# Kernel tuning notes

Hardware: AMD Instinct MI355X
Metric: run time of the kernel (lower is better)

The kernel has to match this reference:

```python
import jax, jax.numpy as jnp
import numpy as np

B, C, H, W = 8, 256, 64, 64
N = 3  # num_param
EPS = 1e-5


def conv2d(x, w, b=None, stride=(1, 1), padding=((0, 0), (0, 0)), dilation=(1, 1), groups=1):
    out = jax.lax.conv_general_dilated(
        x, w, window_strides=stride, padding=padding, rhs_dilation=dilation,
        dimension_numbers=('NCHW', 'OIHW', 'NCHW'), feature_group_count=groups)
    if b is not None:
        out = out + b[None, :, None, None]
    return out


def akconv(x, p_w, p_b, ak_w, ak_gamma, ak_beta):
    b, c, h, w = x.shape
    offset = conv2d(x, p_w, p_b, padding=((1, 1), (1, 1)))  # (b, 2N, h, w)
    # initial kernel offsets p_n for num_param=3: rows [0,0,1], cols [0,1,0]
    p_n = jnp.concatenate([jnp.array([0., 0., 1.]), jnp.array([0., 1., 0.])]).reshape(1, 2 * N, 1, 1)
    gx = jnp.broadcast_to(jnp.arange(h, dtype=x.dtype)[:, None], (h, w))
    gy = jnp.broadcast_to(jnp.arange(w, dtype=x.dtype)[None, :], (h, w))
    p_0 = jnp.concatenate([jnp.tile(gx[None, None], (1, N, 1, 1)),
                           jnp.tile(gy[None, None], (1, N, 1, 1))], axis=1)  # (1, 2N, h, w)
    p = p_0 + p_n + offset                      # (b, 2N, h, w)
    p = jnp.transpose(p, (0, 2, 3, 1))          # (b, h, w, 2N)
    q = jnp.floor(jax.lax.stop_gradient(p))
    q_lt_x = jnp.clip(q[..., :N], 0, h - 1)
    q_lt_y = jnp.clip(q[..., N:], 0, w - 1)
    q_rb_x = jnp.clip(q[..., :N] + 1, 0, h - 1)
    q_rb_y = jnp.clip(q[..., N:] + 1, 0, w - 1)
    px = jnp.clip(p[..., :N], 0, h - 1)
    py = jnp.clip(p[..., N:], 0, w - 1)
    # bilinear weights (b, h, w, N)
    g_lt = (1 + (q_lt_x - px)) * (1 + (q_lt_y - py))
    g_rb = (1 - (q_rb_x - px)) * (1 - (q_rb_y - py))
    g_lb = (1 + (q_lt_x - px)) * (1 - (q_rb_y - py))
    g_rt = (1 - (q_rb_x - px)) * (1 + (q_lt_y - py))

    x_flat = x.reshape(b, c, h * w)

    def gather(qx, qy):
        idx = (qx * w + qy).astype(jnp.int32).reshape(b, -1)  # (b, h*w*N)
        out = jnp.take_along_axis(x_flat, idx[:, None, :], axis=2)
        return out.reshape(b, c, h, w, N)

    x_off = (g_lt[:, None] * gather(q_lt_x, q_lt_y)
             + g_rb[:, None] * gather(q_rb_x, q_rb_y)
             + g_lb[:, None] * gather(q_lt_x, q_rb_y)
             + g_rt[:, None] * gather(q_rb_x, q_lt_y))   # (b, c, h, w, N)
    # rearrange 'b c h w n -> b c (h n) w'
    x_off = jnp.transpose(x_off, (0, 1, 2, 4, 3)).reshape(b, c, h * N, w)
    out = conv2d(x_off, ak_w, None, stride=(N, 1))        # (b, c, h, w)
    # BatchNorm2d in training mode (batch statistics) + SiLU
    mean = out.mean(axis=(0, 2, 3), keepdims=True)
    var = ((out - mean) ** 2).mean(axis=(0, 2, 3), keepdims=True)
    out = (out - mean) / jnp.sqrt(var + EPS) * ak_gamma[None, :, None, None] + ak_beta[None, :, None, None]
    return jax.nn.silu(out)


def lka(x, w0, b0, ws, bs, w1, b1):
    u = x
    attn = conv2d(x, w0, b0, padding=((2, 2), (2, 2)), groups=C)                       # 5x5 depthwise
    attn = conv2d(attn, ws, bs, padding=((9, 9), (9, 9)), dilation=(3, 3), groups=C)   # 7x7 dw, dil 3
    attn = conv2d(attn, w1, b1)                                                        # 1x1
    return u * attn


def setup_inputs() -> dict:
    key = jax.random.key(0)
    ks = jax.random.split(key, 8)
    return {
        'x': jax.random.normal(ks[0], (B, C, H, W), jnp.float32),
        'p_w': jax.random.normal(ks[1], (2 * N, C, 3, 3), jnp.float32) * 0.01,
        'p_b': jnp.zeros((2 * N,), jnp.float32),
        'ak_w': jax.random.normal(ks[2], (C, C, 3, 1), jnp.float32) * 0.05,
        'ak_gamma': jnp.ones((C,), jnp.float32),
        'ak_beta': jnp.zeros((C,), jnp.float32),
        'lka0_w': jax.random.normal(ks[3], (C, 1, 5, 5), jnp.float32) * 0.05,
        'lka0_b': jnp.zeros((C,), jnp.float32),
        'lkas_w': jax.random.normal(ks[4], (C, 1, 7, 7), jnp.float32) * 0.05,
        'lkas_b': jnp.zeros((C,), jnp.float32),
        'lka1_w': jax.random.normal(ks[5], (C, C, 1, 1), jnp.float32) * 0.05,
        'lka1_b': jnp.zeros((C,), jnp.float32),
        'conv_w': jax.random.normal(ks[6], (C, C, 1, 1), jnp.float32) * 0.05,
        'conv_b': jnp.zeros((C,), jnp.float32),
    }


def reference(x, p_w, p_b, ak_w, ak_gamma, ak_beta, lka0_w, lka0_b, lkas_w, lkas_b, lka1_w, lka1_b, conv_w, conv_b):
    res = x
    y = akconv(x, p_w, p_b, ak_w, ak_gamma, ak_beta)
    y = lka(y, lka0_w, lka0_b, lkas_w, lkas_b, lka1_w, lka1_b)
    y = conv2d(y, conv_w, conv_b)
    return y + res
```

## Files before the change

### kernel.cpp

```cpp
#include <hip/hip_runtime.h>
#include <math.h>
#include <stdint.h>

#define B_ 8
#define C_ 256
#define HW_ 4096
#define NPIX 32768
#define NELEM (B_*C_*HW_)

typedef __attribute__((ext_vector_type(8))) short short8;
typedef __attribute__((ext_vector_type(4))) float f32x4;

__device__ __forceinline__ unsigned short f2bf(float f) {
    union { float f; uint32_t u; } v; v.f = f;
    uint32_t r = v.u + 0x7FFFu + ((v.u >> 16) & 1u);
    return (unsigned short)(r >> 16);
}
__device__ __forceinline__ float b2f(unsigned short h) {
    union { uint32_t u; float f; } v; v.u = ((uint32_t)h) << 16; return v.f;
}
__device__ __forceinline__ float silu_f(float v) { return v / (1.f + __expf(-v)); }

__device__ __forceinline__ float4 up4(uint2 v) {
    float4 r;
    r.x = b2f((unsigned short)(v.x & 0xffffu));
    r.y = b2f((unsigned short)(v.x >> 16));
    r.z = b2f((unsigned short)(v.y & 0xffffu));
    r.w = b2f((unsigned short)(v.y >> 16));
    return r;
}

__device__ __forceinline__ void gl2lds16(const void* g, void* l) {
    __builtin_amdgcn_global_load_lds(
        (const __attribute__((address_space(1))) void*)g,
        (__attribute__((address_space(3))) void*)l,
        16, 0, 0);
}

__global__ __launch_bounds__(256) void prep_transpose_kernel(
    const float* __restrict__ akw, const float* __restrict__ l1w,
    const float* __restrict__ cvw, const float* __restrict__ pw,
    unsigned short* __restrict__ wak, unsigned short* __restrict__ wl1,
    unsigned short* __restrict__ wcv, float* __restrict__ pwt,
    const float* __restrict__ x, unsigned short* __restrict__ xt)
{
    __shared__ float tile[64 * 132];
    int blk = blockIdx.x;
    int tid = threadIdx.x;
    if (blk < 1024) {
        int b = blk & 7;
        int rest = blk >> 3;
        int half = rest & 1, i = rest >> 1;
        int bi = b * 64 + i;
        {
            int ci_l = tid >> 6, jj = tid & 63;
            const float* ip = x + ((size_t)b * C_ + half * 128 + ci_l) * HW_ + i * 64 + jj;
            #pragma unroll 4
            for (int it = 0; it < 32; ++it)
                tile[jj * 132 + ci_l + it * 4] = ip[(size_t)it * 4 * HW_];
        }
        __syncthreads();
        {
            int j = tid >> 2, q = tid & 3;
            unsigned short* op = xt + ((size_t)(bi * 64 + j)) * 256 + half * 128 + q * 32;
            const float* tp = &tile[j * 132 + q * 32];
            #pragma unroll
            for (int f = 0; f < 4; ++f) {
                union { unsigned short h[8]; uint4 u; } pk;
                #pragma unroll
                for (int e = 0; e < 8; ++e) pk.h[e] = f2bf(tp[f * 8 + e]);
                *(uint4*)(op + f * 8) = pk.u;
            }
        }
        return;
    }
    int gid = (blk - 1024) * 256 + tid;
    if (gid < 196608) {
        int e = gid & 7;
        int co = (gid >> 3) & 255;
        int q = gid >> 11;
        int kpp = q * 8 + e;
        int n = kpp >> 8, ci = kpp & 255;
        wak[gid] = f2bf(akw[co * 768 + ci * 3 + n]);
    }
    else if (gid < 262144) {
        int g = gid - 196608;
        int e = g & 7, co = (g >> 3) & 255, q = g >> 11;
        wl1[g] = f2bf(l1w[co * 256 + q * 8 + e]);
    }
    else if (gid < 327680) {
        int g = gid - 262144;
        int e = g & 7, co = (g >> 3) & 255, q = g >> 11;
        wcv[g] = f2bf(cvw[co * 256 + q * 8 + e]);
    }
    else if (gid < 346112) {
        int idx = gid - 327680;
        int ci = idx / 72, r = idx - ci * 72;
        int tt = r / 12, t9 = r - tt * 12;
        pwt[idx] = (t9 < 9) ? pw[tt * 2304 + ci * 9 + t9] : 0.f;
    }
}

__global__ __launch_bounds__(256) void offset_s1_kernel(
    const float* __restrict__ x, const float* __restrict__ pwt,
    float* __restrict__ part)
{
    int blk = blockIdx.x;
    int b = blk & 7;
    int rest = blk >> 3;
    int g = rest & 7, i = rest >> 3;
    int bi = b * 64 + i;
    int tid = threadIdx.x;

    __shared__ float tile[6600];

    {
        int cs = tid >> 3, r8 = tid & 7;
        const float* xp = x + ((size_t)b * C_ + g * 32 + cs) * HW_;
        #pragma unroll
        for (int t = 0; t < 6; ++t) {
            int idx = r8 * 6 + t;
            int r = idx >> 4, v4 = idx & 15;
            int ii = i + r - 1;
            float4 val = make_float4(0.f, 0.f, 0.f, 0.f);
            if (ii >= 0 && ii < 64)
                val = *(const float4*)(xp + ii * 64 + v4 * 4);
            int base = (r * 66 + 1 + v4 * 4) * 33 + cs;
            tile[base]      = val.x;  tile[base + 33]  = val.y;
            tile[base + 66] = val.z;  tile[base + 99]  = val.w;
        }
        if (tid < 192) {
            int ci = tid / 6, rem = tid - ci * 6;
            int ki = rem >> 1, side = rem & 1;
            tile[(ki * 66 + side * 65) * 33 + ci] = 0.f;
        }
    }
    __syncthreads();

    int sub = tid >> 4;
    int jq  = tid & 15;

    float acc[6][4];
    #pragma unroll
    for (int tt = 0; tt < 6; ++tt)
        #pragma unroll
        for (int p = 0; p < 4; ++p) acc[tt][p] = 0.f;

    #pragma unroll
    for (int t = 0; t < 2; ++t) {
        int ci = sub + 16 * t;
        float xv[3][6];
        #pragma unroll
        for (int ki = 0; ki < 3; ++ki)
            #pragma unroll
            for (int cc = 0; cc < 6; ++cc)
                xv[ki][cc] = tile[(ki * 66 + jq * 4 + cc) * 33 + ci];
        const float* wp = pwt + (g * 32 + ci) * 72;
        #pragma unroll
        for (int tt = 0; tt < 6; ++tt) {
            float w[9];
            *(float4*)&w[0] = *(const float4*)(wp + tt * 12);
            *(float4*)&w[4] = *(const float4*)(wp + tt * 12 + 4);
            w[8] = wp[tt * 12 + 8];
            #pragma unroll
            for (int ki = 0; ki < 3; ++ki)
                #pragma unroll
                for (int kj = 0; kj < 3; ++kj) {
                    float wgt = w[ki * 3 + kj];
                    #pragma unroll
                    for (int p = 0; p < 4; ++p)
                        acc[tt][p] += wgt * xv[ki][kj + p];
                }
        }
    }

    __syncthreads();
    {
        float* s2 = tile + sub * 387;
        #pragma unroll
        for (int tt = 0; tt < 6; ++tt)
            #pragma unroll
            for (int p = 0; p < 4; ++p)
                s2[tt * 64 + jq * 4 + p] = acc[tt][p];
    }
    __syncthreads();
    size_t pslot = (size_t)bi * 8 + g;
    for (int idx = tid; idx < 384; idx += 256) {
        float s = 0.f;
        #pragma unroll
        for (int sb = 0; sb < 16; ++sb)
            s += tile[sb * 387 + idx];
        part[pslot * 384 + idx] = s;
    }
}

__global__ __launch_bounds__(256) void offset_s2_kernel(
    const float* __restrict__ part, const float* __restrict__ pb,
    int2* __restrict__ tbl_off, float4* __restrict__ tbl_w)
{
    int pix = blockIdx.x * 256 + threadIdx.x;
    int b = pix >> 12, rem = pix & 4095, i = rem >> 6, j = rem & 63;
    int bi = b * 64 + i;
    float v[6];
    #pragma unroll
    for (int tt = 0; tt < 6; ++tt) v[tt] = pb[tt];
    for (int g = 0; g < 8; ++g) {
        const float* pp = part + ((size_t)bi * 8 + g) * 384;
        #pragma unroll
        for (int tt = 0; tt < 6; ++tt) v[tt] += pp[tt * 64 + j];
    }
    const float pnx[3] = {0.f, 0.f, 1.f};
    const float pny[3] = {0.f, 1.f, 0.f};
    #pragma unroll
    for (int n = 0; n < 3; ++n) {
        float px_ = (float)i + pnx[n] + v[n];
        float py_ = (float)j + pny[n] + v[n + 3];
        float qx = floorf(px_), qy = floorf(py_);
        float qlx = fminf(fmaxf(qx,       0.f), 63.f);
        float qly = fminf(fmaxf(qy,       0.f), 63.f);
        float qrx = fminf(fmaxf(qx + 1.f, 0.f), 63.f);
        float qry = fminf(fmaxf(qy + 1.f, 0.f), 63.f);
        float pxc = fminf(fmaxf(px_,      0.f), 63.f);
        float pyc = fminf(fmaxf(py_,      0.f), 63.f);
        float glt = (1.f + (qlx - pxc)) * (1.f + (qly - pyc));
        float grb = (1.f - (qrx - pxc)) * (1.f - (qry - pyc));
        float glb = (1.f + (qlx - pxc)) * (1.f - (qry - pyc));
        float grt = (1.f - (qrx - pxc)) * (1.f + (qly - pyc));
        int ilx = (int)qlx, irx = (int)qrx;
        int ily = (int)qly, iry = (int)qry;
        int c0; float a0, a1, b0, b1;
        if (ily == iry) {
            if (ily == 0) { c0 = 0;  a0 = glt + glb; a1 = 0.f; b0 = grt + grb; b1 = 0.f; }
            else          { c0 = 62; a0 = 0.f; a1 = glt + glb; b0 = 0.f; b1 = grt + grb; }
        } else { c0 = ily; a0 = glt; a1 = glb; b0 = grt; b1 = grb; }
        int oi = (b * 3 + n) * HW_ + i * 64 + j;
        tbl_off[oi] = make_int2(ilx * 64 + c0, irx * 64 + c0);
        tbl_w[oi]   = make_float4(a0, a1, b0, b1);
    }
}

__global__ __launch_bounds__(256) void gather_kernel(
    const unsigned short* __restrict__ xt, const int2* __restrict__ tbl_off,
    const float4* __restrict__ tbl_w, unsigned short* __restrict__ v)
{
    int blk = blockIdx.x;
    int b = blk & 7;
    int rest = blk >> 3;
    int n = rest >> 6, i = rest & 63;
    int bi = b * 64 + i;
    int tid = threadIdx.x;
    int lane = tid & 63, wv = tid >> 6;
    int ci4 = lane * 4;
    const unsigned short* xb = xt + (size_t)b * 1048576;

    __shared__ unsigned short stile[16640];
    int tCloc = ci4 >> 5;
    int kq = (ci4 >> 3) & 3;
    int e  = ci4 & 7;
    unsigned short* sl = &stile[tCloc * 2080 + kq * 520 + e];

    for (int it0 = 0; it0 < 16; it0 += 8) {
        uint2 A8[8], B8[8], C8[8], D8[8];
        float4 w4[8];
        #pragma unroll
        for (int u = 0; u < 8; ++u) {
            int j = wv * 16 + it0 + u;
            int oi = (b * 3 + n) * HW_ + i * 64 + j;
            int2 off = tbl_off[oi];
            w4[u] = tbl_w[oi];
            const unsigned short* p0 = xb + (size_t)off.x * 256 + ci4;
            const unsigned short* p1 = xb + (size_t)off.y * 256 + ci4;
            A8[u] = *(const uint2*)p0;
            B8[u] = *(const uint2*)(p0 + 256);
            C8[u] = *(const uint2*)p1;
            D8[u] = *(const uint2*)(p1 + 256);
        }
        #pragma unroll
        for (int u = 0; u < 8; ++u) {
            int j = wv * 16 + it0 + u;
            float4 A = up4(A8[u]), Bv = up4(B8[u]), Cv = up4(C8[u]), Dv = up4(D8[u]);
            union { unsigned short h[4]; uint2 q; } pk;
            pk.h[0] = f2bf(w4[u].x*A.x + w4[u].y*Bv.x + w4[u].z*Cv.x + w4[u].w*Dv.x);
            pk.h[1] = f2bf(w4[u].x*A.y + w4[u].y*Bv.y + w4[u].z*Cv.y + w4[u].w*Dv.y);
            pk.h[2] = f2bf(w4[u].x*A.z + w4[u].y*Bv.z + w4[u].z*Cv.z + w4[u].w*Dv.z);
            pk.h[3] = f2bf(w4[u].x*A.w + w4[u].y*Bv.w + w4[u].z*Cv.w + w4[u].w*Dv.w);
            *(uint2*)&sl[j * 8] = pk.q;
        }
    }
    __syncthreads();
    unsigned short* vb = v + ((size_t)bi * 24 + n * 8) * 2048;
    int kqW = tid >> 6, jW = tid & 63;
    #pragma unroll
    for (int tc = 0; tc < 8; ++tc) {
        *(uint4*)&vb[tc * 2048 + kqW * 512 + jW * 8] =
            *(const uint4*)&stile[tc * 2080 + kqW * 520 + jW * 8];
    }
}

__global__ __launch_bounds__(256) void ak_mfma_kernel(
    const unsigned short* __restrict__ v, const unsigned short* __restrict__ W,
    unsigned short* __restrict__ yh, float* __restrict__ p1, float* __restrict__ p2)
{
    int pid = blockIdx.x;
    int mt2 = (pid >> 3) & 1;
    int rest = (pid & 7) | ((pid >> 4) << 3);
    int b = rest & 7, i = rest >> 3;
    int co0 = mt2 * 128;
    int tid = threadIdx.x;
    int wv = tid >> 6, lane = tid & 63;
    int quad = lane >> 4, l15 = lane & 15;
    __shared__ __align__(16) unsigned short sA[4096];
    __shared__ __align__(16) unsigned short sB[2048];

    const unsigned short* vP = v + (size_t)(b * 64 + i) * 24 * 2048;
    int cS = tid & 127, hS = tid >> 7;

    f32x4 acc[2][4];
    #pragma unroll
    for (int mt = 0; mt < 2; ++mt)
        #pragma unroll
        for (int nt = 0; nt < 4; ++nt) acc[mt][nt] = (f32x4){0.f, 0.f, 0.f, 0.f};

    for (int t = 0; t < 24; ++t) {
        #pragma unroll
        for (int s = 0; s < 2; ++s) {
            int chunk = hS * 2 + s;
            gl2lds16(W + ((size_t)(t * 4 + chunk) * 256 + co0 + cS) * 8,
                     &sA[(chunk * 128 + cS) * 8]);
        }
        gl2lds16(vP + (size_t)t * 2048 + tid * 8, &sB[tid * 8]);
        __syncthreads();
        short8 af[2], bf[4];
        #pragma unroll
        for (int mt = 0; mt < 2; ++mt)
            af[mt] = *(const short8*)&sA[(quad * 128 + wv * 32 + mt * 16 + l15) * 8];
        #pragma unroll
        for (int nt = 0; nt < 4; ++nt)
            bf[nt] = *(const short8*)&sB[(quad * 64 + nt * 16 + l15) * 8];
        #pragma unroll
        for (int mt = 0; mt < 2; ++mt)
            #pragma unroll
            for (int nt = 0; nt < 4; ++nt)
                acc[mt][nt] = __builtin_amdgcn_mfma_f32_16x16x32_bf16(
                    af[mt], bf[nt], acc[mt][nt], 0, 0, 0);
        __syncthreads();
    }
    #pragma unroll
    for (int mt = 0; mt < 2; ++mt) {
        #pragma unroll
        for (int r = 0; r < 4; ++r) {
            int co = co0 + wv * 32 + mt * 16 + quad * 4 + r;
            size_t base = ((size_t)b * C_ + co) * HW_ + i * 64;
            float s1 = 0.f, s2 = 0.f;
            #pragma unroll
            for (int nt = 0; nt < 4; ++nt) {
                float val = acc[mt][nt][r];
                s1 += val; s2 += val * val;
                yh[base + nt * 16 + l15] = f2bf(val);
            }
            #pragma unroll
            for (int m = 1; m < 16; m <<= 1) {
                s1 += __shfl_xor(s1, m); s2 += __shfl_xor(s2, m);
            }
            if (l15 == 0) { p1[co * 512 + rest] = s1; p2[co * 512 + rest] = s2; }
        }
    }
}

__global__ __launch_bounds__(256) void bn_stats_kernel(
    const float* __restrict__ p1, const float* __restrict__ p2,
    const float* __restrict__ gamma, const float* __restrict__ beta,
    float* __restrict__ ss)
{
    int co = blockIdx.x, tid = threadIdx.x;
    float a = p1[co * 512 + tid] + p1[co * 512 + 256 + tid];
    float q = p2[co * 512 + tid] + p2[co * 512 + 256 + tid];
    __shared__ float r1[256], r2[256];
    r1[tid] = a; r2[tid] = q; __syncthreads();
    for (int st = 128; st > 0; st >>= 1) {
        if (tid < st) { r1[tid] += r1[tid + st]; r2[tid] += r2[tid + st]; }
        __syncthreads();
    }
    if (tid == 0) {
        const float inv_n = 1.f / (float)NPIX;
        float m = r1[0] * inv_n;
        float var = r2[0] * inv_n - m * m;
        float sc = gamma[co] * rsqrtf(var + 1e-5f);
        ss[co] = sc; ss[256 + co] = beta[co] - m * sc;
    }
}

__global__ __launch_bounds__(256) void dw5_fused_kernel(
    const unsigned short* __restrict__ in, const float* __restrict__ ss,
    const float* __restrict__ w, const float* __restrict__ bias,
    unsigned short* __restrict__ out)
{
    int blkI = blockIdx.x;
    int b = blkI & 7, c = blkI >> 3;
    int bc = b * 256 + c;
    int tid = threadIdx.x;
    __shared__ float tile[68 * 68];
    float sc = ss[c], sh = ss[256 + c];
    const unsigned short* ip = in + (size_t)bc * HW_;
    for (int s = tid; s < 68 * 68; s += 256) {
        int r = s / 68, cc = s - r * 68;
        int ii = r - 2, jj = cc - 2;
        float vv = 0.f;
        if (ii >= 0 && ii < 64 && jj >= 0 && jj < 64) {
            float t = b2f(ip[ii * 64 + jj]) * sc + sh;
            vv = silu_f(t);
        }
        tile[s] = vv;
    }
    float wr[25];
    #pragma unroll
    for (int t = 0; t < 25; ++t) wr[t] = w[c * 25 + t];
    float bv = bias[c];
    __syncthreads();

    int jb = tid & 3, row = tid >> 2;
    int j0 = jb * 16;
    float acc[16];
    #pragma unroll
    for (int j = 0; j < 16; ++j) acc[j] = bv;
    #pragma unroll
    for (int di = 0; di < 5; ++di) {
        const float* tp = &tile[(row + di) * 68 + j0];
        float vv[20];
        #pragma unroll
        for (int q = 0; q < 5; ++q)
            *(float4*)&vv[q * 4] = *(const float4*)(tp + q * 4);
        #pragma unroll
        for (int dj = 0; dj < 5; ++dj) {
            float wv = wr[di * 5 + dj];
            #pragma unroll
            for (int j = 0; j < 16; ++j)
                acc[j] += wv * vv[dj + j];
        }
    }
    unsigned short* op = out + (size_t)bc * HW_ + row * 64 + j0;
    union { unsigned short h[8]; uint4 u; } pk;
    #pragma unroll
    for (int half = 0; half < 2; ++half) {
        #pragma unroll
        for (int j = 0; j < 8; ++j) pk.h[j] = f2bf(acc[half * 8 + j]);
        *(uint4*)&op[half * 8] = pk.u;
    }
}

__global__ __launch_bounds__(256) void dw7d3_kernel(
    const unsigned short* __restrict__ in, const float* __restrict__ w,
    const float* __restrict__ bias, unsigned short* __restrict__ out)
{
    int blkI = blockIdx.x;
    int b = blkI & 7, c = blkI >> 3;
    int bc = b * 256 + c;
    int tid = threadIdx.x;
    __shared__ float tile[82 * 84];
    const unsigned short* ip = in + (size_t)bc * HW_;
    for (int s = tid; s < 82 * 84; s += 256) {
        int r = s / 84, cc = s - r * 84;
        int ii = r - 9, jj = cc - 9;
        float vv = 0.f;
        if (ii >= 0 && ii < 64 && jj >= 0 && jj < 64) vv = b2f(ip[ii * 64 + jj]);
        tile[s] = vv;
    }
    float wr[49];
    #pragma unroll
    for (int t = 0; t < 49; ++t) wr[t] = w[c * 49 + t];
    float bv = bias[c];
    __syncthreads();

    int jb = tid & 3, row = tid >> 2;
    int j0 = jb * 16;
    float acc[16];
    #pragma unroll
    for (int j = 0; j < 16; ++j) acc[j] = bv;
    #pragma unroll
    for (int di = 0; di < 7; ++di) {
        const float* tp = &tile[(row + 3 * di) * 84 + j0];
        float vv[36];
        #pragma unroll
        for (int q = 0; q < 9; ++q)
            *(float4*)&vv[q * 4] = *(const float4*)(tp + q * 4);
        #pragma unroll
        for (int dj = 0; dj < 7; ++dj) {
            float wv = wr[di * 7 + dj];
            #pragma unroll
            for (int j = 0; j < 16; ++j)
                acc[j] += wv * vv[3 * dj + j];
        }
    }
    unsigned short* op = out + (size_t)bc * HW_ + row * 64 + j0;
    union { unsigned short h[8]; uint4 u; } pk;
    #pragma unroll
    for (int half = 0; half < 2; ++half) {
        #pragma unroll
        for (int j = 0; j < 8; ++j) pk.h[j] = f2bf(acc[half * 8 + j]);
        *(uint4*)&op[half * 8] = pk.u;
    }
}

__global__ __launch_bounds__(256) void gemm_fused_kernel(
    const unsigned short* __restrict__ in,
    const unsigned short* __restrict__ W0, const float* __restrict__ bias0,
    const unsigned short* __restrict__ W1, const float* __restrict__ bias1,
    const unsigned short* __restrict__ auxh, const float* __restrict__ ss,
    const float* __restrict__ auxf, float* __restrict__ out_f)
{
    int blk = blockIdx.x;
    int b = blk & 7, i = blk >> 3;
    int tid = threadIdx.x;
    int wv = tid >> 6, lane = tid & 63;
    int quad = lane >> 4, l15 = lane & 15;
    __shared__ __align__(16) unsigned short sA[8192];
    __shared__ __align__(16) unsigned short sB[2048];
    __shared__ __align__(16) unsigned short mid[16384];
    int pixS = tid & 63, kqS = tid >> 6;

    const unsigned short* bp = in + ((size_t)b * C_) * HW_ + i * 64 + pixS;

    f32x4 acc[4][4];
    #pragma unroll
    for (int mt = 0; mt < 4; ++mt)
        #pragma unroll
        for (int nt = 0; nt < 4; ++nt) acc[mt][nt] = (f32x4){0.f, 0.f, 0.f, 0.f};

    for (int t = 0; t < 8; ++t) {
        #pragma unroll
        for (int s = 0; s < 4; ++s)
            gl2lds16(W0 + ((size_t)(t * 4 + s) * 256 + tid) * 8, &sA[(s * 256 + tid) * 8]);
        {
            const unsigned short* p = bp + (size_t)(t * 32 + kqS * 8) * HW_;
            union { unsigned short h[8]; uint4 u; } hb;
            #pragma unroll
            for (int jj = 0; jj < 8; ++jj) hb.h[jj] = p[(size_t)jj * HW_];
            *(uint4*)&sB[(kqS * 64 + pixS) * 8] = hb.u;
        }
        __syncthreads();
        short8 af[4], bf[4];
        #pragma unroll
        for (int mt = 0; mt < 4; ++mt)
            af[mt] = *(const short8*)&sA[(quad * 256 + wv * 64 + mt * 16 + l15) * 8];
        #pragma unroll
        for (int nt = 0; nt < 4; ++nt)
            bf[nt] = *(const short8*)&sB[(quad * 64 + nt * 16 + l15) * 8];
        #pragma unroll
        for (int mt = 0; mt < 4; ++mt)
            #pragma unroll
            for (int nt = 0; nt < 4; ++nt)
                acc[mt][nt] = __builtin_amdgcn_mfma_f32_16x16x32_bf16(
                    af[mt], bf[nt], acc[mt][nt], 0, 0, 0);
        __syncthreads();
    }
    #pragma unroll
    for (int mt = 0; mt < 4; ++mt) {
        #pragma unroll
        for (int r = 0; r < 4; ++r) {
            int co = wv * 64 + mt * 16 + quad * 4 + r;
            float bco = bias0[co];
            size_t base = ((size_t)b * C_ + co) * HW_ + i * 64;
            float sc = ss[co], sh = ss[256 + co];
            #pragma unroll
            for (int nt = 0; nt < 4; ++nt) {
                int col = nt * 16 + l15;
                float o = acc[mt][nt][r] + bco;
                float u = silu_f(b2f(auxh[base + col]) * sc + sh);
                mid[((co >> 3) * 64 + col) * 8 + (co & 7)] = f2bf(o * u);
            }
        }
    }
    #pragma unroll
    for (int mt = 0; mt < 4; ++mt)
        #pragma unroll
        for (int nt = 0; nt < 4; ++nt) acc[mt][nt] = (f32x4){0.f, 0.f, 0.f, 0.f};
    for (int t = 0; t < 8; ++t) {
        #pragma unroll
        for (int s = 0; s < 4; ++s)
            gl2lds16(W1 + ((size_t)(t * 4 + s) * 256 + tid) * 8, &sA[(s * 256 + tid) * 8]);
        __syncthreads();
        short8 af[4], bf[4];
        #pragma unroll
        for (int mt = 0; mt < 4; ++mt)
            af[mt] = *(const short8*)&sA[(quad * 256 + wv * 64 + mt * 16 + l15) * 8];
        #pragma unroll
        for (int nt = 0; nt < 4; ++nt)
            bf[nt] = *(const short8*)&mid[((t * 4 + quad) * 64 + nt * 16 + l15) * 8];
        #pragma unroll
        for (int mt = 0; mt < 4; ++mt)
            #pragma unroll
            for (int nt = 0; nt < 4; ++nt)
                acc[mt][nt] = __builtin_amdgcn_mfma_f32_16x16x32_bf16(
                    af[mt], bf[nt], acc[mt][nt], 0, 0, 0);
        __syncthreads();
    }
    #pragma unroll
    for (int mt = 0; mt < 4; ++mt) {
        #pragma unroll
        for (int r = 0; r < 4; ++r) {
            int co = wv * 64 + mt * 16 + quad * 4 + r;
            float bco = bias1[co];
            size_t base = ((size_t)b * C_ + co) * HW_ + i * 64;
            #pragma unroll
            for (int nt = 0; nt < 4; ++nt) {
                int col = nt * 16 + l15;
                out_f[base + col] = acc[mt][nt][r] + bco + auxf[base + col];
            }
        }
    }
}

extern "C" void kernel_launch(void* const* d_in, const int* in_sizes, int n_in,
                              void* d_out, int out_size, void* d_ws, size_t ws_size,
                              hipStream_t stream) {
    const float* x     = (const float*)d_in[0];
    const float* p_w   = (const float*)d_in[1];
    const float* p_b   = (const float*)d_in[2];
    const float* ak_w  = (const float*)d_in[3];
    const float* ak_g  = (const float*)d_in[4];
    const float* ak_b  = (const float*)d_in[5];
    const float* l0_w  = (const float*)d_in[6];
    const float* l0_b  = (const float*)d_in[7];
    const float* ls_w  = (const float*)d_in[8];
    const float* ls_b  = (const float*)d_in[9];
    const float* l1_w  = (const float*)d_in[10];
    const float* l1_b  = (const float*)d_in[11];
    const float* cv_w  = (const float*)d_in[12];
    const float* cv_b  = (const float*)d_in[13];
    float* out = (float*)d_out;

    char* w = (char*)d_ws;
    int2*   tbl_off = (int2*)w;
    float4* tbl_w   = (float4*)(w + 786432);
    unsigned short* wak = (unsigned short*)(w + 2359296);
    unsigned short* wl1 = (unsigned short*)(w + 2752512);
    unsigned short* wcv = (unsigned short*)(w + 2883584);
    float* p1 = (float*)(w + 3014656);
    float* p2 = (float*)(w + 3538944);
    float* ss = (float*)(w + 4063232);
    float* pwt = (float*)(w + 4065280);
    unsigned short* xt = (unsigned short*)(w + 4194304);
    unsigned short* ybh    = (unsigned short*)(w + 4194304);
    unsigned short* dw5out = (unsigned short*)(w + 20971520);
    float* part = (float*)(w + 37748736);
    unsigned short* attn   = (unsigned short*)(w + 37748736);
    unsigned short* v      = (unsigned short*)(w + 44040192);

    prep_transpose_kernel<<<2376, 256, 0, stream>>>(ak_w, l1_w, cv_w, p_w,
                                                    wak, wl1, wcv, pwt, x, xt);
    offset_s1_kernel<<<4096, 256, 0, stream>>>(x, pwt, part);
    offset_s2_kernel<<<128, 256, 0, stream>>>(part, p_b, tbl_off, tbl_w);
    gather_kernel<<<1536, 256, 0, stream>>>(xt, tbl_off, tbl_w, v);
    ak_mfma_kernel<<<1024, 256, 0, stream>>>(v, wak, ybh, p1, p2);
    bn_stats_kernel<<<256, 256, 0, stream>>>(p1, p2, ak_g, ak_b, ss);
    dw5_fused_kernel<<<2048, 256, 0, stream>>>(ybh, ss, l0_w, l0_b, dw5out);
    dw7d3_kernel<<<2048, 256, 0, stream>>>(dw5out, ls_w, ls_b, attn);
    gemm_fused_kernel<<<512, 256, 0, stream>>>(attn, wl1, l1_b, wcv, cv_b, ybh, ss, x, out);
}
```

Measured before the change: 266.8 us.

## Fuse offset table computation into gather and halve pixel tile in fused GEMM

Removes the offset_s2 kernel and its global offset/weight tables. Each gather block now computes its 64 bilinear offsets and weights into shared memory before gathering, which saves one launch and a global round trip but repeats some partial-sum reads per block. Separately, the fused double-GEMM kernel now covers 32 pixels per block instead of 64, doubling the grid to 1024 blocks with less LDS and fewer accumulators per block. The trade-off is that the weight matrices are reloaded twice as often.

```diff
diff --git a/kernel.cpp b/kernel.cpp
--- a/kernel.cpp
+++ b/kernel.cpp
@@ -194,27 +194,36 @@
     }
 }
 
-__global__ __launch_bounds__(256) void offset_s2_kernel(
-    const float* __restrict__ part, const float* __restrict__ pb,
-    int2* __restrict__ tbl_off, float4* __restrict__ tbl_w)
-{
-    int pix = blockIdx.x * 256 + threadIdx.x;
-    int b = pix >> 12, rem = pix & 4095, i = rem >> 6, j = rem & 63;
+__global__ __launch_bounds__(256) void gather_kernel(
+    const unsigned short* __restrict__ xt, const float* __restrict__ part,
+    const float* __restrict__ pb, unsigned short* __restrict__ v)
+{
+    int blk = blockIdx.x;
+    int b = blk & 7;
+    int rest = blk >> 3;
+    int n = rest >> 6, i = rest & 63;
     int bi = b * 64 + i;
-    float v[6];
-    #pragma unroll
-    for (int tt = 0; tt < 6; ++tt) v[tt] = pb[tt];
-    for (int g = 0; g < 8; ++g) {
-        const float* pp = part + ((size_t)bi * 8 + g) * 384;
-        #pragma unroll
-        for (int tt = 0; tt < 6; ++tt) v[tt] += pp[tt * 64 + j];
-    }
-    const float pnx[3] = {0.f, 0.f, 1.f};
-    const float pny[3] = {0.f, 1.f, 0.f};
-    #pragma unroll
-    for (int n = 0; n < 3; ++n) {
-        float px_ = (float)i + pnx[n] + v[n];
-        float py_ = (float)j + pny[n] + v[n + 3];
+    int tid = threadIdx.x;
+    int lane = tid & 63, wv = tid >> 6;
+    int ci4 = lane * 4;
+    const unsigned short* xb = xt + (size_t)b * 1048576;
+
+    __shared__ unsigned short stile[16640];
+    __shared__ int2 loff[64];
+    __shared__ float4 lw[64];
+
+    if (tid < 64) {
+        int j = tid;
+        float vn = pb[n], vn3 = pb[n + 3];
+        for (int g = 0; g < 8; ++g) {
+            const float* pp = part + ((size_t)bi * 8 + g) * 384;
+            vn  += pp[n * 64 + j];
+            vn3 += pp[(n + 3) * 64 + j];
+        }
+        float pnx_n = (n == 2) ? 1.f : 0.f;
+        float pny_n = (n == 1) ? 1.f : 0.f;
+        float px_ = (float)i + pnx_n + vn;
+        float py_ = (float)j + pny_n + vn3;
         float qx = floorf(px_), qy = floorf(py_);
         float qlx = fminf(fmaxf(qx,       0.f), 63.f);
         float qly = fminf(fmaxf(qy,       0.f), 63.f);
@@ -233,27 +242,11 @@
             if (ily == 0) { c0 = 0;  a0 = glt + glb; a1 = 0.f; b0 = grt + grb; b1 = 0.f; }
             else          { c0 = 62; a0 = 0.f; a1 = glt + glb; b0 = 0.f; b1 = grt + grb; }
         } else { c0 = ily; a0 = glt; a1 = glb; b0 = grt; b1 = grb; }
-        int oi = (b * 3 + n) * HW_ + i * 64 + j;
-        tbl_off[oi] = make_int2(ilx * 64 + c0, irx * 64 + c0);
-        tbl_w[oi]   = make_float4(a0, a1, b0, b1);
-    }
-}
-
-__global__ __launch_bounds__(256) void gather_kernel(
-    const unsigned short* __restrict__ xt, const int2* __restrict__ tbl_off,
-    const float4* __restrict__ tbl_w, unsigned short* __restrict__ v)
-{
-    int blk = blockIdx.x;
-    int b = blk & 7;
-    int rest = blk >> 3;
-    int n = rest >> 6, i = rest & 63;
-    int bi = b * 64 + i;
-    int tid = threadIdx.x;
-    int lane = tid & 63, wv = tid >> 6;
-    int ci4 = lane * 4;
-    const unsigned short* xb = xt + (size_t)b * 1048576;
-
-    __shared__ unsigned short stile[16640];
+        loff[j] = make_int2(ilx * 64 + c0, irx * 64 + c0);
+        lw[j]   = make_float4(a0, a1, b0, b1);
+    }
+    __syncthreads();
+
     int tCloc = ci4 >> 5;
     int kq = (ci4 >> 3) & 3;
     int e  = ci4 & 7;
@@ -265,9 +258,8 @@
         #pragma unroll
         for (int u = 0; u < 8; ++u) {
             int j = wv * 16 + it0 + u;
-            int oi = (b * 3 + n) * HW_ + i * 64 + j;
-            int2 off = tbl_off[oi];
-            w4[u] = tbl_w[oi];
+            int2 off = loff[j];
+            w4[u] = lw[j];
             const unsigned short* p0 = xb + (size_t)off.x * 256 + ci4;
             const unsigned short* p1 = xb + (size_t)off.y * 256 + ci4;
             A8[u] = *(const uint2*)p0;
@@ -509,46 +501,49 @@
     const float* __restrict__ auxf, float* __restrict__ out_f)
 {
     int blk = blockIdx.x;
-    int b = blk & 7, i = blk >> 3;
+    int b = blk & 7;
+    int rest = blk >> 3;
+    int half = rest & 1, i = rest >> 1;
+    int pix0 = i * 64 + half * 32;
     int tid = threadIdx.x;
     int wv = tid >> 6, lane = tid & 63;
     int quad = lane >> 4, l15 = lane & 15;
     __shared__ __align__(16) unsigned short sA[8192];
-    __shared__ __align__(16) unsigned short sB[2048];
-    __shared__ __align__(16) unsigned short mid[16384];
-    int pixS = tid & 63, kqS = tid >> 6;
-
-    const unsigned short* bp = in + ((size_t)b * C_) * HW_ + i * 64 + pixS;
-
-    f32x4 acc[4][4];
+    __shared__ __align__(16) unsigned short sB[1024];
+    __shared__ __align__(16) unsigned short mid[8192];
+    int pxS = tid & 31, kqS = (tid >> 5) & 3;
+
+    const unsigned short* bp = in + ((size_t)b * C_) * HW_ + pix0 + pxS;
+
+    f32x4 acc[4][2];
     #pragma unroll
     for (int mt = 0; mt < 4; ++mt)
         #pragma unroll
-        for (int nt = 0; nt < 4; ++nt) acc[mt][nt] = (f32x4){0.f, 0.f, 0.f, 0.f};
+        for (int nt = 0; nt < 2; ++nt) acc[mt][nt] = (f32x4){0.f, 0.f, 0.f, 0.f};
 
     for (int t = 0; t < 8; ++t) {
         #pragma unroll
         for (int s = 0; s < 4; ++s)
             gl2lds16(W0 + ((size_t)(t * 4 + s) * 256 + tid) * 8, &sA[(s * 256 + tid) * 8]);
-        {
+        if (tid < 128) {
             const unsigned short* p = bp + (size_t)(t * 32 + kqS * 8) * HW_;
             union { unsigned short h[8]; uint4 u; } hb;
             #pragma unroll
             for (int jj = 0; jj < 8; ++jj) hb.h[jj] = p[(size_t)jj * HW_];
-            *(uint4*)&sB[(kqS * 64 + pixS) * 8] = hb.u;
-        }
-        __syncthreads();
-        short8 af[4], bf[4];
+            *(uint4*)&sB[(kqS * 32 + pxS) * 8] = hb.u;
+        }
+        __syncthreads();
+        short8 af[4], bf[2];
         #pragma unroll
         for (int mt = 0; mt < 4; ++mt)
             af[mt] = *(const short8*)&sA[(quad * 256 + wv * 64 + mt * 16 + l15) * 8];
         #pragma unroll
-        for (int nt = 0; nt < 4; ++nt)
-            bf[nt] = *(const short8*)&sB[(quad * 64 + nt * 16 + l15) * 8];
+        for (int nt = 0; nt < 2; ++nt)
+            bf[nt] = *(const short8*)&sB[(quad * 32 + nt * 16 + l15) * 8];
         #pragma unroll
         for (int mt = 0; mt < 4; ++mt)
             #pragma unroll
-            for (int nt = 0; nt < 4; ++nt)
+            for (int nt = 0; nt < 2; ++nt)
                 acc[mt][nt] = __builtin_amdgcn_mfma_f32_16x16x32_bf16(
                     af[mt], bf[nt], acc[mt][nt], 0, 0, 0);
         __syncthreads();
@@ -559,37 +554,37 @@
         for (int r = 0; r < 4; ++r) {
             int co = wv * 64 + mt * 16 + quad * 4 + r;
             float bco = bias0[co];
-            size_t base = ((size_t)b * C_ + co) * HW_ + i * 64;
+            size_t base = ((size_t)b * C_ + co) * HW_ + pix0;
             float sc = ss[co], sh = ss[256 + co];
             #pragma unroll
-            for (int nt = 0; nt < 4; ++nt) {
+            for (int nt = 0; nt < 2; ++nt) {
                 int col = nt * 16 + l15;
                 float o = acc[mt][nt][r] + bco;
                 float u = silu_f(b2f(auxh[base + col]) * sc + sh);
-                mid[((co >> 3) * 64 + col) * 8 + (co & 7)] = f2bf(o * u);
+                mid[((co >> 3) * 32 + col) * 8 + (co & 7)] = f2bf(o * u);
             }
         }
     }
     #pragma unroll
     for (int mt = 0; mt < 4; ++mt)
         #pragma unroll
-        for (int nt = 0; nt < 4; ++nt) acc[mt][nt] = (f32x4){0.f, 0.f, 0.f, 0.f};
+        for (int nt = 0; nt < 2; ++nt) acc[mt][nt] = (f32x4){0.f, 0.f, 0.f, 0.f};
     for (int t = 0; t < 8; ++t) {
         #pragma unroll
         for (int s = 0; s < 4; ++s)
             gl2lds16(W1 + ((size_t)(t * 4 + s) * 256 + tid) * 8, &sA[(s * 256 + tid) * 8]);
         __syncthreads();
-        short8 af[4], bf[4];
+        short8 af[4], bf[2];
         #pragma unroll
         for (int mt = 0; mt < 4; ++mt)
             af[mt] = *(const short8*)&sA[(quad * 256 + wv * 64 + mt * 16 + l15) * 8];
         #pragma unroll
-        for (int nt = 0; nt < 4; ++nt)
-            bf[nt] = *(const short8*)&mid[((t * 4 + quad) * 64 + nt * 16 + l15) * 8];
+        for (int nt = 0; nt < 2; ++nt)
+            bf[nt] = *(const short8*)&mid[((t * 4 + quad) * 32 + nt * 16 + l15) * 8];
         #pragma unroll
         for (int mt = 0; mt < 4; ++mt)
             #pragma unroll
-            for (int nt = 0; nt < 4; ++nt)
+            for (int nt = 0; nt < 2; ++nt)
                 acc[mt][nt] = __builtin_amdgcn_mfma_f32_16x16x32_bf16(
                     af[mt], bf[nt], acc[mt][nt], 0, 0, 0);
         __syncthreads();
@@ -600,9 +595,9 @@
         for (int r = 0; r < 4; ++r) {
             int co = wv * 64 + mt * 16 + quad * 4 + r;
             float bco = bias1[co];
-            size_t base = ((size_t)b * C_ + co) * HW_ + i * 64;
-            #pragma unroll
-            for (int nt = 0; nt < 4; ++nt) {
+            size_t base = ((size_t)b * C_ + co) * HW_ + pix0;
+            #pragma unroll
+            for (int nt = 0; nt < 2; ++nt) {
                 int col = nt * 16 + l15;
                 out_f[base + col] = acc[mt][nt][r] + bco + auxf[base + col];
             }
@@ -630,8 +625,6 @@
     float* out = (float*)d_out;
 
     char* w = (char*)d_ws;
-    int2*   tbl_off = (int2*)w;
-    float4* tbl_w   = (float4*)(w + 786432);
     unsigned short* wak = (unsigned short*)(w + 2359296);
     unsigned short* wl1 = (unsigned short*)(w + 2752512);
     unsigned short* wcv = (unsigned short*)(w + 2883584);
@@ -649,11 +642,10 @@
     prep_transpose_kernel<<<2376, 256, 0, stream>>>(ak_w, l1_w, cv_w, p_w,
                                                     wak, wl1, wcv, pwt, x, xt);
     offset_s1_kernel<<<4096, 256, 0, stream>>>(x, pwt, part);
-    offset_s2_kernel<<<128, 256, 0, stream>>>(part, p_b, tbl_off, tbl_w);
-    gather_kernel<<<1536, 256, 0, stream>>>(xt, tbl_off, tbl_w, v);
+    gather_kernel<<<1536, 256, 0, stream>>>(xt, part, p_b, v);
     ak_mfma_kernel<<<1024, 256, 0, stream>>>(v, wak, ybh, p1, p2);
     bn_stats_kernel<<<256, 256, 0, stream>>>(p1, p2, ak_g, ak_b, ss);
     dw5_fused_kernel<<<2048, 256, 0, stream>>>(ybh, ss, l0_w, l0_b, dw5out);
     dw7d3_kernel<<<2048, 256, 0, stream>>>(dw5out, ls_w, ls_b, attn);
-    gemm_fused_kernel<<<512, 256, 0, stream>>>(attn, wl1, l1_b, wcv, cv_b, ybh, ss, x, out);
-}
+    gemm_fused_kernel<<<1024, 256, 0, stream>>>(attn, wl1, l1_b, wcv, cv_b, ybh, ss, x, out);
+}
```

Result: faster. 257.6 us (median of 2 runs) (-3.5%).
